# Kernel optimization log

Hardware: AMD Instinct MI355X
Metric: run time of the kernel (lower is better)

The kernel has to match this reference:

```python
import math
import jax, jax.numpy as jnp
import numpy as np

T = 4096          # sequence length
H = 2048          # hidden_size
I = 8192          # intermediate_size = 4*H
LAYER_ID = 1
N_LAYERS = 24
EPS = 1e-5        # layer_norm_epsilon


def setup_inputs() -> dict:
    key = jax.random.key(0)
    ks = jax.random.split(key, 8)
    s = 1.0 / math.sqrt(H)
    si = 1.0 / math.sqrt(I)
    r0 = LAYER_ID / (N_LAYERS - 1)          # ratio_0_to_1
    r1 = 1.0 - LAYER_ID / N_LAYERS          # ratio_1_to_almost_0
    h = jnp.arange(H, dtype=jnp.float32)
    x = h / H
    time_decay = -5.0 + 8.0 * (h / (H - 1)) ** (0.7 + 1.3 * r0)
    zigzag = 0.5 * ((jnp.arange(1, H + 1) % 3).astype(jnp.float32) - 1.0)
    time_first = jnp.full((H,), math.log(0.3), jnp.float32) + zigzag
    tm_key = x ** r1
    tm_value = tm_key + 0.3 * r0
    tm_recep = x ** (0.5 * r1)
    return {
        "hidden": jax.random.normal(ks[0], (T, H), jnp.float32),
        "att_sx": jnp.zeros((H,), jnp.float32),
        "att_aa": jnp.zeros((H,), jnp.float32),
        "att_bb": jnp.zeros((H,), jnp.float32),
        "att_pp": jnp.full((H,), -1e30, jnp.float32),  # log-space -inf init
        "ffd_sx": jnp.zeros((H,), jnp.float32),
        "ln1_scale": jnp.ones((H,), jnp.float32),
        "ln1_bias": jnp.zeros((H,), jnp.float32),
        "ln2_scale": jnp.ones((H,), jnp.float32),
        "ln2_bias": jnp.zeros((H,), jnp.float32),
        "time_decay": time_decay.astype(jnp.float32),
        "time_first": time_first,
        "tm_key": tm_key.astype(jnp.float32),
        "tm_value": tm_value.astype(jnp.float32),
        "tm_recep": tm_recep.astype(jnp.float32),
        "Wk": jax.random.normal(ks[1], (H, H), jnp.float32) * s,
        "Wv": jax.random.normal(ks[2], (H, H), jnp.float32) * s,
        "Wr": jax.random.normal(ks[3], (H, H), jnp.float32) * s,
        "Wo": jax.random.normal(ks[4], (H, H), jnp.float32) * s,
        "ffn_tm_key": (x ** r1).astype(jnp.float32),
        "ffn_tm_recep": (x ** (0.5 * r1)).astype(jnp.float32),
        "Wfk": jax.random.normal(ks[5], (H, I), jnp.float32) * s,
        "Wfr": jax.random.normal(ks[6], (H, H), jnp.float32) * s,
        "Wfv": jax.random.normal(ks[7], (I, H), jnp.float32) * si,
    }


def _ln(x, scale, bias):
    mu = jnp.mean(x, axis=-1, keepdims=True)
    var = jnp.mean(jnp.square(x - mu), axis=-1, keepdims=True)
    return (x - mu) * jax.lax.rsqrt(var + EPS) * scale + bias


def _block(hidden, att_sx, att_aa, att_bb, att_pp, ffd_sx,
           ln1_scale, ln1_bias, ln2_scale, ln2_bias,
           time_decay, time_first, tm_key, tm_value, tm_recep,
           Wk, Wv, Wr, Wo, ffn_tm_key, ffn_tm_recep, Wfk, Wfr, Wfv):
    # ---- attention (WKV) sub-block ----
    x1 = _ln(hidden, ln1_scale, ln1_bias)               # [T,H]
    c_x = jnp.concatenate((att_sx[None, :], x1[:-1, :]), axis=0)  # token shift
    kx = x1 * tm_key + c_x * (1.0 - tm_key)
    vx = x1 * tm_value + c_x * (1.0 - tm_value)
    rx = x1 * tm_recep + c_x * (1.0 - tm_recep)
    r = jax.nn.sigmoid(rx @ Wr)                         # [T,H]
    k = kx @ Wk
    v = vx @ Wv
    w_decay = -jnp.exp(time_decay)                      # [H]

    def step(carry, kv):
        aa, bb, pp = carry
        kk, vv = kv
        ww = time_first + kk
        p = jnp.maximum(pp, ww)
        e1 = jnp.exp(pp - p)
        e2 = jnp.exp(ww - p)
        out_t = (e1 * aa + e2 * vv) / (e1 * bb + e2)
        ww2 = w_decay + pp
        p2 = jnp.maximum(ww2, kk)
        e1b = jnp.exp(ww2 - p2)
        e2b = jnp.exp(kk - p2)
        return (e1b * aa + e2b * vv, e1b * bb + e2b, p2), out_t

    (aa, bb, pp), cx = jax.lax.scan(step, (att_aa, att_bb, att_pp), (k, v))
    attention = x1 + (r * cx) @ Wo                      # inner residual (as in source)
    hidden2 = hidden + attention

    # ---- feed-forward (channel-mix) sub-block ----
    x2 = _ln(hidden2, ln2_scale, ln2_bias)
    sx2 = jnp.concatenate((ffd_sx[None, :], x2[:-1, :]), axis=0)
    fk = x2 * ffn_tm_key + sx2 * (1.0 - ffn_tm_key)
    fr = x2 * ffn_tm_recep + sx2 * (1.0 - ffn_tm_recep)
    rr = jax.nn.sigmoid(fr @ Wfr)
    kk2 = jnp.square(jax.nn.relu(fk @ Wfk))             # [T,I]
    ffn = rr * (kk2 @ Wfv)
    out = hidden2 + ffn
    return out, x1[-1, :], aa, bb, pp, x2[-1, :]


def reference(hidden, att_sx, att_aa, att_bb, att_pp, ffd_sx,
              ln1_scale, ln1_bias, ln2_scale, ln2_bias,
              time_decay, time_first, tm_key, tm_value, tm_recep,
              Wk, Wv, Wr, Wo, ffn_tm_key, ffn_tm_recep, Wfk, Wfr, Wfv):
    return _block(hidden, att_sx, att_aa, att_bb, att_pp, ffd_sx,
                  ln1_scale, ln1_bias, ln2_scale, ln2_bias,
                  time_decay, time_first, tm_key, tm_value, tm_recep,
                  Wk, Wv, Wr, Wo, ffn_tm_key, ffn_tm_recep, Wfk, Wfr, Wfv)
```

## Files before the change

kernel.cpp:

```cpp
#include <hip/hip_runtime.h>

#define T_SEQ 4096
#define HD 2048
#define ID 8192
#define LN_EPS 1e-5f
#define NCH 64
#define CHL 64
#define CHSZ ((size_t)NCH * HD)

typedef __attribute__((ext_vector_type(4))) float f32x4;
typedef __attribute__((ext_vector_type(8))) short short8;
typedef __attribute__((ext_vector_type(4))) unsigned short ushort4v;

#define GLB(p) ((const __attribute__((address_space(1))) void*)(p))
#define LDSP(p) ((__attribute__((address_space(3))) void*)(p))

__device__ __forceinline__ unsigned short f2bf(float f) {
  union { float f; unsigned int u; } x; x.f = f;
  unsigned int r = x.u + 0x7fffu + ((x.u >> 16) & 1u);
  return (unsigned short)(r >> 16);
}
__device__ __forceinline__ float bf2f(unsigned short u) {
  union { unsigned int i; float f; } x; x.i = ((unsigned int)u) << 16;
  return x.f;
}

__global__ void k_wt(const float* __restrict__ W, unsigned short* __restrict__ Wt,
                     int Nfull, int k_base, int n_base, int Kout) {
  __shared__ float tile[32][33];
  int tx = threadIdx.x, ty = threadIdx.y;
  int n0 = blockIdx.x * 32, k0 = blockIdx.y * 32;
#pragma unroll
  for (int j = 0; j < 4; ++j) {
    int k = ty + 8 * j;
    tile[k][tx] = W[(size_t)(k_base + k0 + k) * Nfull + n_base + n0 + tx];
  }
  __syncthreads();
#pragma unroll
  for (int j = 0; j < 4; ++j) {
    int n = ty + 8 * j;
    Wt[(size_t)(n0 + n) * Kout + k0 + tx] = f2bf(tile[tx][n]);
  }
}

__global__ void k_ln(const float* __restrict__ x, const float* __restrict__ sc,
                     const float* __restrict__ bi, unsigned short* __restrict__ y,
                     float* __restrict__ lastrow) {
  int row = blockIdx.x, tid = threadIdx.x;
  const float* xr = x + (size_t)row * HD;
  f32x4 v0 = *(const f32x4*)(xr + tid * 4);
  f32x4 v1 = *(const f32x4*)(xr + 1024 + tid * 4);
  float s = 0.f, s2 = 0.f;
#pragma unroll
  for (int q = 0; q < 4; ++q) { s += v0[q] + v1[q]; s2 += v0[q] * v0[q] + v1[q] * v1[q]; }
#pragma unroll
  for (int o = 32; o; o >>= 1) { s += __shfl_xor(s, o); s2 += __shfl_xor(s2, o); }
  __shared__ float red[8];
  int wv = tid >> 6;
  if ((tid & 63) == 0) { red[wv] = s; red[4 + wv] = s2; }
  __syncthreads();
  if (tid == 0) {
    float a = red[0] + red[1] + red[2] + red[3];
    float b = red[4] + red[5] + red[6] + red[7];
    float mu = a * (1.f / HD);
    float var = b * (1.f / HD) - mu * mu;
    red[0] = mu; red[1] = rsqrtf(var + LN_EPS);
  }
  __syncthreads();
  float mu = red[0], rs = red[1];
  f32x4 s0 = *(const f32x4*)(sc + tid * 4), s1 = *(const f32x4*)(sc + 1024 + tid * 4);
  f32x4 b0 = *(const f32x4*)(bi + tid * 4), b1 = *(const f32x4*)(bi + 1024 + tid * 4);
  float o0[4], o1[4];
  ushort4v y0, y1;
#pragma unroll
  for (int q = 0; q < 4; ++q) {
    o0[q] = (v0[q] - mu) * rs * s0[q] + b0[q];
    o1[q] = (v1[q] - mu) * rs * s1[q] + b1[q];
    y0[q] = f2bf(o0[q]); y1[q] = f2bf(o1[q]);
  }
  unsigned short* yr = y + (size_t)row * HD;
  *(ushort4v*)(yr + tid * 4) = y0;
  *(ushort4v*)(yr + 1024 + tid * 4) = y1;
  if (row == T_SEQ - 1) {
#pragma unroll
    for (int q = 0; q < 4; ++q) {
      lastrow[tid * 4 + q] = o0[q];
      lastrow[1024 + tid * 4 + q] = o1[q];
    }
  }
}

__global__ void k_mix_att(const unsigned short* __restrict__ x1, const float* __restrict__ sx,
                          const float* __restrict__ tk, const float* __restrict__ tv,
                          const float* __restrict__ tr,
                          unsigned short* __restrict__ kx, unsigned short* __restrict__ vx,
                          unsigned short* __restrict__ rx) {
  size_t idx = ((size_t)blockIdx.x * 256 + threadIdx.x) * 4;
  int h = (int)(idx & (HD - 1));
  ushort4v xu = *(const ushort4v*)(x1 + idx);
  f32x4 x, c;
#pragma unroll
  for (int q = 0; q < 4; ++q) x[q] = bf2f(xu[q]);
  if (idx >= HD) {
    ushort4v cu = *(const ushort4v*)(x1 + idx - HD);
#pragma unroll
    for (int q = 0; q < 4; ++q) c[q] = bf2f(cu[q]);
  } else {
    c = *(const f32x4*)(sx + h);
  }
  f32x4 a = *(const f32x4*)(tk + h);
  f32x4 b = *(const f32x4*)(tv + h);
  f32x4 r = *(const f32x4*)(tr + h);
  ushort4v ok, ov, orr;
#pragma unroll
  for (int q = 0; q < 4; ++q) {
    ok[q] = f2bf(x[q] * a[q] + c[q] * (1.f - a[q]));
    ov[q] = f2bf(x[q] * b[q] + c[q] * (1.f - b[q]));
    orr[q] = f2bf(x[q] * r[q] + c[q] * (1.f - r[q]));
  }
  *(ushort4v*)(kx + idx) = ok;
  *(ushort4v*)(vx + idx) = ov;
  *(ushort4v*)(rx + idx) = orr;
}

__global__ void k_mix_ffn(const unsigned short* __restrict__ x2, const float* __restrict__ sx,
                          const float* __restrict__ tk, const float* __restrict__ tr,
                          unsigned short* __restrict__ fk, unsigned short* __restrict__ fr) {
  size_t idx = ((size_t)blockIdx.x * 256 + threadIdx.x) * 4;
  int h = (int)(idx & (HD - 1));
  ushort4v xu = *(const ushort4v*)(x2 + idx);
  f32x4 x, c;
#pragma unroll
  for (int q = 0; q < 4; ++q) x[q] = bf2f(xu[q]);
  if (idx >= HD) {
    ushort4v cu = *(const ushort4v*)(x2 + idx - HD);
#pragma unroll
    for (int q = 0; q < 4; ++q) c[q] = bf2f(cu[q]);
  } else {
    c = *(const f32x4*)(sx + h);
  }
  f32x4 a = *(const f32x4*)(tk + h);
  f32x4 r = *(const f32x4*)(tr + h);
  ushort4v ok, orr;
#pragma unroll
  for (int q = 0; q < 4; ++q) {
    ok[q] = f2bf(x[q] * a[q] + c[q] * (1.f - a[q]));
    orr[q] = f2bf(x[q] * r[q] + c[q] * (1.f - r[q]));
  }
  *(ushort4v*)(fk + idx) = ok;
  *(ushort4v*)(fr + idx) = orr;
}

__global__ void k_scan1(const unsigned short* __restrict__ kb,
                        const unsigned short* __restrict__ vb,
                        const float* __restrict__ td, float* __restrict__ scr) {
  int c = blockIdx.x >> 3;
  int h = (blockIdx.x & 7) * 256 + threadIdx.x;
  float wd = -__expf(td[h]);
  float a = 0.f, b = 0.f, p = -1e30f;
  size_t base = (size_t)c * CHL * HD + h;
#pragma unroll 4
  for (int u = 0; u < CHL; ++u) {
    float kk = bf2f(kb[base]), vv = bf2f(vb[base]);
    base += HD;
    float ww2 = wd + p;
    float p2 = fmaxf(ww2, kk);
    float e1 = __expf(ww2 - p2), e2 = __expf(kk - p2);
    a = e1 * a + e2 * vv;
    b = e1 * b + e2;
    p = p2;
  }
  size_t i = (size_t)c * HD + h;
  scr[i] = a;
  scr[CHSZ + i] = b;
  scr[2 * CHSZ + i] = p;
}

__global__ void k_scan2(const float* __restrict__ scr, float* __restrict__ stscr,
                        const float* __restrict__ aa0, const float* __restrict__ bb0,
                        const float* __restrict__ pp0, const float* __restrict__ td,
                        float* __restrict__ st) {
  int h = blockIdx.x * 256 + threadIdx.x;
  float aa = aa0[h], bb = bb0[h], pp = pp0[h];
  float wdL = -__expf(td[h]) * (float)CHL;
  for (int c = 0; c < NCH; ++c) {
    size_t i = (size_t)c * HD + h;
    stscr[i] = aa;
    stscr[CHSZ + i] = bb;
    stscr[2 * CHSZ + i] = pp;
    float ca = scr[i], cb = scr[CHSZ + i], cp = scr[2 * CHSZ + i];
    float ww2 = wdL + pp;
    float p2 = fmaxf(ww2, cp);
    float e1 = __expf(ww2 - p2), e2 = __expf(cp - p2);
    aa = e1 * aa + e2 * ca;
    bb = e1 * bb + e2 * cb;
    pp = p2;
  }
  st[HD + h] = aa;
  st[2 * HD + h] = bb;
  st[3 * HD + h] = pp;
}

__global__ void k_scan3(const unsigned short* __restrict__ kb,
                        const unsigned short* __restrict__ vb,
                        const unsigned short* __restrict__ rb,
                        const float* __restrict__ tf_, const float* __restrict__ td,
                        const float* __restrict__ stscr, unsigned short* __restrict__ rcx) {
  int c = blockIdx.x >> 3;
  int h = (blockIdx.x & 7) * 256 + threadIdx.x;
  size_t i0 = (size_t)c * HD + h;
  float aa = stscr[i0], bb = stscr[CHSZ + i0], pp = stscr[2 * CHSZ + i0];
  float tf = tf_[h];
  float wd = -__expf(td[h]);
  size_t base = (size_t)c * CHL * HD + h;
#pragma unroll 4
  for (int u = 0; u < CHL; ++u) {
    float kk = bf2f(kb[base]), vv = bf2f(vb[base]), rv = bf2f(rb[base]);
    float ww = tf + kk;
    float p = fmaxf(pp, ww);
    float e1 = __expf(pp - p), e2 = __expf(ww - p);
    float cx = (e1 * aa + e2 * vv) / (e1 * bb + e2);
    rcx[base] = f2bf(rv * cx);
    float ww2 = wd + pp;
    float p2 = fmaxf(ww2, kk);
    float e1b = __expf(ww2 - p2), e2b = __expf(kk - p2);
    aa = e1b * aa + e2b * vv;
    bb = e1b * bb + e2b;
    pp = p2;
    base += HD;
  }
}

#define MFMA_Q(mh, nh, bset)                                                   \
  _Pragma("unroll") for (int i_ = 0; i_ < 4; ++i_)                             \
  _Pragma("unroll") for (int j_ = 0; j_ < 2; ++j_)                             \
  _Pragma("unroll") for (int ks_ = 0; ks_ < 2; ++ks_)                          \
    acc[(mh)*4 + i_][(nh)*2 + j_] = __builtin_amdgcn_mfma_f32_16x16x32_bf16(   \
        aS[i_ * 2 + ks_], bset[j_ * 2 + ks_], acc[(mh)*4 + i_][(nh)*2 + j_], 0, 0, 0);

#define RD_A(mh)                                                               \
  { const char* pa_ = Ab + arow0 + (mh)*8192;                                  \
    aS[0] = *(const short8*)(pa_ + 0 * 2048 + swz0);                           \
    aS[1] = *(const short8*)(pa_ + 0 * 2048 + swz1);                           \
    aS[2] = *(const short8*)(pa_ + 1 * 2048 + swz0);                           \
    aS[3] = *(const short8*)(pa_ + 1 * 2048 + swz1);                           \
    aS[4] = *(const short8*)(pa_ + 2 * 2048 + swz0);                           \
    aS[5] = *(const short8*)(pa_ + 2 * 2048 + swz1);                           \
    aS[6] = *(const short8*)(pa_ + 3 * 2048 + swz0);                           \
    aS[7] = *(const short8*)(pa_ + 3 * 2048 + swz1); }

#define RD_B(arr, nh)                                                          \
  { const char* pb_ = Bb + brow0 + (nh)*4096;                                  \
    arr[0] = *(const short8*)(pb_ + 0 * 2048 + swz0);                          \
    arr[1] = *(const short8*)(pb_ + 0 * 2048 + swz1);                          \
    arr[2] = *(const short8*)(pb_ + 1 * 2048 + swz0);                          \
    arr[3] = *(const short8*)(pb_ + 1 * 2048 + swz1); }

template <int EPI>
__global__ __launch_bounds__(512, 2) void k_gemm256(
    const unsigned short* __restrict__ A, const unsigned short* __restrict__ A1,
    const unsigned short* __restrict__ A2,
    const unsigned short* __restrict__ Bt, const unsigned short* __restrict__ Bt1,
    const unsigned short* __restrict__ Bt2,
    int M, int N, int K, int lda,
    unsigned short* __restrict__ Cb, unsigned short* __restrict__ Cb1,
    unsigned short* __restrict__ Cb2) {
  if (blockIdx.z == 1) { A = A1; Bt = Bt1; Cb = Cb1; }
  else if (blockIdx.z == 2) { A = A2; Bt = Bt2; Cb = Cb2; }
  __shared__ char lds[131072];
  int tid = threadIdx.x;
  int wid = tid >> 6, lane = tid & 63;
  int row_l = lane & 15, kg = lane >> 4;
  int warp_m = wid >> 2, warp_n = wid & 3;
  int m0 = blockIdx.x * 256, n0 = blockIdx.y * 256;

  f32x4 acc[8][4];
#pragma unroll
  for (int i = 0; i < 8; ++i)
#pragma unroll
    for (int j = 0; j < 4; ++j)
#pragma unroll
      for (int q = 0; q < 4; ++q) acc[i][j][q] = 0.f;

  int srow = tid >> 3;
  int schunk = (tid & 7) ^ (srow & 7);
  const unsigned short* Asrc = A + (size_t)(m0 + srow) * lda + schunk * 8;
  const unsigned short* Bsrc = Bt + (size_t)(n0 + srow) * K + schunk * 8;
  char* ldsw = lds + wid * 1024;

  auto STAGE_TILE = [&](int d, int kt) {
#pragma unroll
    for (int h = 0; h < 2; ++h) {
      const unsigned short* s = Asrc + (size_t)(h * 128) * lda + kt;
      char* dst = ldsw + d * 65536 + h * 16384;
      __builtin_amdgcn_global_load_lds(GLB(s), LDSP(dst), 16, 0, 0);
      __builtin_amdgcn_global_load_lds(GLB(s + (size_t)64 * lda), LDSP(dst + 8192), 16, 0, 0);
    }
#pragma unroll
    for (int h = 0; h < 2; ++h) {
      const unsigned short* s = Bsrc + (size_t)(h * 128) * K + kt;
      char* dst = ldsw + d * 65536 + 32768 + h * 16384;
      __builtin_amdgcn_global_load_lds(GLB(s), LDSP(dst), 16, 0, 0);
      __builtin_amdgcn_global_load_lds(GLB(s + (size_t)64 * K), LDSP(dst + 8192), 16, 0, 0);
    }
  };

  int swz0 = ((kg) ^ (row_l & 7)) << 4;
  int swz1 = ((4 + kg) ^ (row_l & 7)) << 4;
  int arow0 = (warp_m * 128 + row_l) * 128;
  int brow0 = (warp_n * 64 + row_l) * 128;

  short8 aS[8], b0[4], b1[4];
  int nt = K >> 6;
  STAGE_TILE(0, 0);

#pragma unroll 1
  for (int t = 0; t < nt; ++t) {
    int d = t & 1;
    const char* Ab = lds + d * 65536;
    const char* Bb = lds + d * 65536 + 32768;
    bool pre = (t + 1 < nt);
    if (pre) {
      STAGE_TILE(d ^ 1, (t + 1) << 6);
      asm volatile("s_waitcnt vmcnt(8)" ::: "memory");
    } else {
      asm volatile("s_waitcnt vmcnt(0)" ::: "memory");
    }
    __builtin_amdgcn_s_barrier();
    RD_A(0)
    RD_B(b0, 0)
    asm volatile("s_waitcnt lgkmcnt(0)" ::: "memory");
    __builtin_amdgcn_s_setprio(1);
    MFMA_Q(0, 0, b0)
    __builtin_amdgcn_s_setprio(0);
    __builtin_amdgcn_s_barrier();
    RD_B(b1, 1)
    asm volatile("s_waitcnt lgkmcnt(0)" ::: "memory");
    __builtin_amdgcn_s_setprio(1);
    MFMA_Q(0, 1, b1)
    __builtin_amdgcn_s_setprio(0);
    __builtin_amdgcn_s_barrier();
    RD_A(1)
    asm volatile("s_waitcnt lgkmcnt(0)" ::: "memory");
    __builtin_amdgcn_s_setprio(1);
    MFMA_Q(1, 1, b1)
    __builtin_amdgcn_s_setprio(0);
    __builtin_amdgcn_s_barrier();
    __builtin_amdgcn_s_setprio(1);
    MFMA_Q(1, 0, b0)
    __builtin_amdgcn_s_setprio(0);
    __builtin_amdgcn_s_barrier();
  }

#pragma unroll
  for (int i = 0; i < 8; ++i) {
#pragma unroll
    for (int j = 0; j < 4; ++j) {
#pragma unroll
      for (int q = 0; q < 4; ++q) {
        int r = m0 + warp_m * 128 + i * 16 + kg * 4 + q;
        int c = n0 + warp_n * 64 + j * 16 + row_l;
        size_t idx = (size_t)r * N + c;
        float val = acc[i][j][q];
        if (EPI == 2) { float t2 = val > 0.f ? val * val : 0.f; Cb[idx] = f2bf(t2); }
        if (EPI == 8) {
          float o = (blockIdx.z == 2) ? 1.f / (1.f + __expf(-val)) : val;
          Cb[idx] = f2bf(o);
        }
      }
    }
  }
}

template <int EPI>
__global__ __launch_bounds__(256) void k_gemm(
    const unsigned short* __restrict__ A, const unsigned short* __restrict__ Bt,
    int M, int N, int K, int lda, float* __restrict__ C,
    unsigned short* __restrict__ Cb, const float* __restrict__ E0,
    const unsigned short* __restrict__ E1b, const unsigned short* __restrict__ E0b) {
  __shared__ unsigned short As[3][128 * 32];
  __shared__ unsigned short Bs[3][128 * 32];
  int tid = threadIdx.x;
  int wave = tid >> 6, lane = tid & 63;
  int row_l = lane & 15, kg = lane >> 4;
  int m0 = blockIdx.x * 128, n0 = blockIdx.y * 128;
  int wm = (wave >> 1) * 64, wn = (wave & 1) * 64;
  f32x4 acc[4][4];
#pragma unroll
  for (int i = 0; i < 4; ++i)
#pragma unroll
    for (int j = 0; j < 4; ++j)
#pragma unroll
      for (int q = 0; q < 4; ++q) acc[i][j][q] = 0.f;

  int trow = tid >> 2, tcol = (tid & 3) * 8;
  const unsigned short* Ag = A + (size_t)(m0 + trow) * lda + tcol;
  const unsigned short* Bg = Bt + (size_t)(n0 + trow) * K + tcol;
  size_t rhalfA = (size_t)64 * lda;
  size_t rhalfB = (size_t)64 * K;
  int woff = wave * 1024;
  int nk = K >> 5;

  auto STAGE = [&](int t, int b) {
    int kt = t * 32;
    char* ad = (char*)As + b * 8192 + woff;
    char* bd = (char*)Bs + b * 8192 + woff;
    __builtin_amdgcn_global_load_lds(GLB(Ag + kt), LDSP(ad), 16, 0, 0);
    __builtin_amdgcn_global_load_lds(GLB(Ag + rhalfA + kt), LDSP(ad + 4096), 16, 0, 0);
    __builtin_amdgcn_global_load_lds(GLB(Bg + kt), LDSP(bd), 16, 0, 0);
    __builtin_amdgcn_global_load_lds(GLB(Bg + rhalfB + kt), LDSP(bd + 4096), 16, 0, 0);
  };

  STAGE(0, 0);
  STAGE(1, 1);
  int buf = 0;
  for (int t = 0; t < nk; ++t) {
    if (t + 2 < nk) {
      int b2 = buf + 2; if (b2 >= 3) b2 -= 3;
      STAGE(t + 2, b2);
      asm volatile("s_waitcnt vmcnt(8)" ::: "memory");
    } else if (t + 1 < nk) {
      asm volatile("s_waitcnt vmcnt(4)" ::: "memory");
    } else {
      asm volatile("s_waitcnt vmcnt(0)" ::: "memory");
    }
    __builtin_amdgcn_s_barrier();
    const unsigned short* Ab = As[buf];
    const unsigned short* Bb = Bs[buf];
    short8 af[4], bfv[4];
#pragma unroll
    for (int i = 0; i < 4; ++i)
      af[i] = *(const short8*)(Ab + (wm + i * 16 + row_l) * 32 + kg * 8);
#pragma unroll
    for (int j = 0; j < 4; ++j)
      bfv[j] = *(const short8*)(Bb + (wn + j * 16 + row_l) * 32 + kg * 8);
    __builtin_amdgcn_s_setprio(1);
#pragma unroll
    for (int i = 0; i < 4; ++i)
#pragma unroll
      for (int j = 0; j < 4; ++j)
        acc[i][j] = __builtin_amdgcn_mfma_f32_16x16x32_bf16(af[i], bfv[j], acc[i][j], 0, 0, 0);
    __builtin_amdgcn_s_setprio(0);
    asm volatile("s_waitcnt lgkmcnt(0)" ::: "memory");
    __builtin_amdgcn_s_barrier();
    ++buf; if (buf >= 3) buf -= 3;
  }

#pragma unroll
  for (int i = 0; i < 4; ++i) {
#pragma unroll
    for (int j = 0; j < 4; ++j) {
#pragma unroll
      for (int q = 0; q < 4; ++q) {
        int r = m0 + wm + i * 16 + kg * 4 + q;
        int c = n0 + wn + j * 16 + row_l;
        size_t idx = (size_t)r * N + c;
        float val = acc[i][j][q];
        if (EPI == 3) C[idx] = val + E0[idx] + bf2f(E1b[idx]);
        if (EPI == 6) Cb[idx] = f2bf(1.f / (1.f + __expf(-val)));
        if (EPI == 7) C[idx] += bf2f(E0b[idx]) * val;
      }
    }
  }
}

extern "C" void kernel_launch(void* const* d_in, const int* in_sizes, int n_in,
                              void* d_out, int out_size, void* d_ws, size_t ws_size,
                              hipStream_t stream) {
  (void)in_sizes; (void)n_in; (void)out_size; (void)ws_size;
  const float* hidden     = (const float*)d_in[0];
  const float* att_sx     = (const float*)d_in[1];
  const float* att_aa     = (const float*)d_in[2];
  const float* att_bb     = (const float*)d_in[3];
  const float* att_pp     = (const float*)d_in[4];
  const float* ffd_sx     = (const float*)d_in[5];
  const float* ln1_s      = (const float*)d_in[6];
  const float* ln1_b      = (const float*)d_in[7];
  const float* ln2_s      = (const float*)d_in[8];
  const float* ln2_b      = (const float*)d_in[9];
  const float* time_decay = (const float*)d_in[10];
  const float* time_first = (const float*)d_in[11];
  const float* tm_key     = (const float*)d_in[12];
  const float* tm_value   = (const float*)d_in[13];
  const float* tm_recep   = (const float*)d_in[14];
  const float* Wk         = (const float*)d_in[15];
  const float* Wv         = (const float*)d_in[16];
  const float* Wr         = (const float*)d_in[17];
  const float* Wo         = (const float*)d_in[18];
  const float* ffn_tm_key = (const float*)d_in[19];
  const float* ffn_tm_rec = (const float*)d_in[20];
  const float* Wfk        = (const float*)d_in[21];
  const float* Wfr        = (const float*)d_in[22];
  const float* Wfv        = (const float*)d_in[23];
  float* out = (float*)d_out;
  float* st = out + (size_t)T_SEQ * HD;

  const size_t MB8 = (size_t)HD * HD * 2;
  const size_t PG = (size_t)T_SEQ * HD * 2;
  char* w = (char*)d_ws;
  unsigned short* s0 = (unsigned short*)(w);
  unsigned short* s1 = (unsigned short*)(w + MB8);
  unsigned short* s2 = (unsigned short*)(w + 2 * MB8);
  unsigned short* s3 = (unsigned short*)(w + 3 * MB8);
  char* pA = w + 4 * MB8;
  char* pB = pA + PG;
  char* pC = pB + PG;
  char* pD = pC + PG;
  char* pE = pD + PG;
  char* pF = pE + PG;

  unsigned short* kx   = (unsigned short*)pA;
  unsigned short* vx   = (unsigned short*)pB;
  unsigned short* rx   = (unsigned short*)pC;
  unsigned short* kbf  = (unsigned short*)pD;
  unsigned short* x1bf = (unsigned short*)pE;
  unsigned short* vbf  = (unsigned short*)pF;
  unsigned short* rbf  = (unsigned short*)out;
  unsigned short* rcx  = (unsigned short*)pC;
  unsigned short* x2bf = (unsigned short*)pD;
  unsigned short* fk   = (unsigned short*)pF;
  unsigned short* fr   = (unsigned short*)pB;
  unsigned short* rr   = (unsigned short*)pA;
  unsigned short* kk2  = (unsigned short*)pB;
  float* scr   = (float*)s0;
  float* stscr = (float*)s1;

  dim3 tb(32, 8);
  dim3 wg64(HD / 32, HD / 32);
  dim3 gg(T_SEQ / 128, HD / 128);

  k_wt<<<wg64, tb, 0, stream>>>(Wk, s0, HD, 0, 0, HD);
  k_wt<<<wg64, tb, 0, stream>>>(Wv, s1, HD, 0, 0, HD);
  k_wt<<<wg64, tb, 0, stream>>>(Wr, s2, HD, 0, 0, HD);
  k_wt<<<wg64, tb, 0, stream>>>(Wo, s3, HD, 0, 0, HD);
  k_ln<<<T_SEQ, 256, 0, stream>>>(hidden, ln1_s, ln1_b, x1bf, st);
  k_mix_att<<<T_SEQ * HD / 1024, 256, 0, stream>>>(x1bf, att_sx, tm_key, tm_value, tm_recep,
                                                   kx, vx, rx);
  k_gemm256<8><<<dim3(T_SEQ / 256, HD / 256, 3), 512, 0, stream>>>(
      kx, vx, rx, s0, s1, s2, T_SEQ, HD, HD, HD, kbf, vbf, rbf);
  k_scan1<<<NCH * 8, 256, 0, stream>>>(kbf, vbf, time_decay, scr);
  k_scan2<<<HD / 256, 256, 0, stream>>>(scr, stscr, att_aa, att_bb, att_pp, time_decay, st);
  k_scan3<<<NCH * 8, 256, 0, stream>>>(kbf, vbf, rbf, time_first, time_decay, stscr, rcx);
  k_gemm<3><<<gg, 256, 0, stream>>>(rcx, s3, T_SEQ, HD, HD, HD, out, nullptr,
                                    hidden, x1bf, nullptr);

  k_ln<<<T_SEQ, 256, 0, stream>>>(out, ln2_s, ln2_b, x2bf, st + 4 * HD);
  k_mix_ffn<<<T_SEQ * HD / 1024, 256, 0, stream>>>(x2bf, ffd_sx, ffn_tm_key, ffn_tm_rec,
                                                   fk, fr);
  k_wt<<<wg64, tb, 0, stream>>>(Wfr, s3, HD, 0, 0, HD);
  k_gemm<6><<<gg, 256, 0, stream>>>(fr, s3, T_SEQ, HD, HD, HD, nullptr, rr,
                                    nullptr, nullptr, nullptr);
  for (int q = 0; q < 4; ++q)
    k_wt<<<wg64, tb, 0, stream>>>(Wfk, s0 + (size_t)q * 2048 * 2048, ID, 0, q * 2048, HD);
  k_gemm256<2><<<dim3(T_SEQ / 256, ID / 256), 512, 0, stream>>>(
      fk, nullptr, nullptr, s0, nullptr, nullptr, T_SEQ, ID, HD, HD,
      kk2, nullptr, nullptr);
  for (int q = 0; q < 4; ++q)
    k_wt<<<dim3(HD / 32, HD / 32), tb, 0, stream>>>(Wfv, s0 + (size_t)q * 2048, HD,
                                                    q * 2048, 0, ID);
  k_gemm<7><<<gg, 256, 0, stream>>>(kk2, s0, T_SEQ, HD, ID, ID, out, nullptr,
                                    nullptr, nullptr, rr);
}
```

Baseline: 736.2 us.

## Replace 128x128 GEMM with 128x256 tile, 512-thread, swizzled LDS variant

The three N=2048 GEMMs (attention output, FFN receptance, FFN value) move to a new kernel that uses 128x256 output tiles with 8 waves and K-steps of 64. It double-buffers in place of triple-buffering and applies an XOR swizzle to the LDS layout to avoid bank conflicts, reusing the RD_A/RD_B/MFMA_Q macros from the 256 kernel. The larger tile raises arithmetic intensity per LDS load, but halves the grid to 256 blocks, which may leave some of the 256 CUs underused or unevenly loaded. The bigger LDS footprint (96KB) also limits occupancy to one block per CU.

After: 674.7 us. 8.4% less time.

```diff
diff --git a/kernel.cpp b/kernel.cpp
--- a/kernel.cpp
+++ b/kernel.cpp
@@ -373,18 +373,18 @@
 }
 
 template <int EPI>
-__global__ __launch_bounds__(256) void k_gemm(
+__global__ __launch_bounds__(512) void k_gemmB(
     const unsigned short* __restrict__ A, const unsigned short* __restrict__ Bt,
     int M, int N, int K, int lda, float* __restrict__ C,
     unsigned short* __restrict__ Cb, const float* __restrict__ E0,
     const unsigned short* __restrict__ E1b, const unsigned short* __restrict__ E0b) {
-  __shared__ unsigned short As[3][128 * 32];
-  __shared__ unsigned short Bs[3][128 * 32];
+  __shared__ char lds[98304];
   int tid = threadIdx.x;
-  int wave = tid >> 6, lane = tid & 63;
+  int wid = tid >> 6, lane = tid & 63;
   int row_l = lane & 15, kg = lane >> 4;
-  int m0 = blockIdx.x * 128, n0 = blockIdx.y * 128;
-  int wm = (wave >> 1) * 64, wn = (wave & 1) * 64;
+  int warp_m = wid >> 2, warp_n = wid & 3;
+  int m0 = blockIdx.x * 128, n0 = blockIdx.y * 256;
+
   f32x4 acc[4][4];
 #pragma unroll
   for (int i = 0; i < 4; ++i)
@@ -393,57 +393,57 @@
 #pragma unroll
       for (int q = 0; q < 4; ++q) acc[i][j][q] = 0.f;
 
-  int trow = tid >> 2, tcol = (tid & 3) * 8;
-  const unsigned short* Ag = A + (size_t)(m0 + trow) * lda + tcol;
-  const unsigned short* Bg = Bt + (size_t)(n0 + trow) * K + tcol;
-  size_t rhalfA = (size_t)64 * lda;
-  size_t rhalfB = (size_t)64 * K;
-  int woff = wave * 1024;
-  int nk = K >> 5;
-
-  auto STAGE = [&](int t, int b) {
-    int kt = t * 32;
-    char* ad = (char*)As + b * 8192 + woff;
-    char* bd = (char*)Bs + b * 8192 + woff;
-    __builtin_amdgcn_global_load_lds(GLB(Ag + kt), LDSP(ad), 16, 0, 0);
-    __builtin_amdgcn_global_load_lds(GLB(Ag + rhalfA + kt), LDSP(ad + 4096), 16, 0, 0);
-    __builtin_amdgcn_global_load_lds(GLB(Bg + kt), LDSP(bd), 16, 0, 0);
-    __builtin_amdgcn_global_load_lds(GLB(Bg + rhalfB + kt), LDSP(bd + 4096), 16, 0, 0);
+  int srow = tid >> 3;
+  int schunk = (tid & 7) ^ (srow & 7);
+  const unsigned short* Asrc = A + (size_t)(m0 + srow) * lda + schunk * 8;
+  const unsigned short* Bsrc = Bt + (size_t)(n0 + srow) * K + schunk * 8;
+  int wsw = wid * 1024;
+
+  auto STAGE_TILE = [&](int d, int kt) {
+    char* base = lds + d * 49152;
+    __builtin_amdgcn_global_load_lds(GLB(Asrc + kt), LDSP(base + wsw), 16, 0, 0);
+    __builtin_amdgcn_global_load_lds(GLB(Asrc + (size_t)64 * lda + kt),
+                                     LDSP(base + 8192 + wsw), 16, 0, 0);
+#pragma unroll
+    for (int h = 0; h < 4; ++h)
+      __builtin_amdgcn_global_load_lds(GLB(Bsrc + (size_t)(h * 64) * K + kt),
+                                       LDSP(base + 16384 + h * 8192 + wsw), 16, 0, 0);
   };
 
-  STAGE(0, 0);
-  STAGE(1, 1);
-  int buf = 0;
-  for (int t = 0; t < nk; ++t) {
-    if (t + 2 < nk) {
-      int b2 = buf + 2; if (b2 >= 3) b2 -= 3;
-      STAGE(t + 2, b2);
-      asm volatile("s_waitcnt vmcnt(8)" ::: "memory");
-    } else if (t + 1 < nk) {
-      asm volatile("s_waitcnt vmcnt(4)" ::: "memory");
+  int swz0 = ((kg) ^ (row_l & 7)) << 4;
+  int swz1 = ((4 + kg) ^ (row_l & 7)) << 4;
+  int arow0 = (warp_m * 64 + row_l) * 128;
+  int brow0 = (warp_n * 64 + row_l) * 128;
+
+  short8 aS[8], b0[4], b1[4];
+  int nt = K >> 6;
+  STAGE_TILE(0, 0);
+
+#pragma unroll 1
+  for (int t = 0; t < nt; ++t) {
+    int d = t & 1;
+    const char* Ab = lds + d * 49152;
+    const char* Bb = lds + d * 49152 + 16384;
+    if (t + 1 < nt) {
+      STAGE_TILE(d ^ 1, (t + 1) << 6);
+      asm volatile("s_waitcnt vmcnt(6)" ::: "memory");
     } else {
       asm volatile("s_waitcnt vmcnt(0)" ::: "memory");
     }
     __builtin_amdgcn_s_barrier();
-    const unsigned short* Ab = As[buf];
-    const unsigned short* Bb = Bs[buf];
-    short8 af[4], bfv[4];
-#pragma unroll
-    for (int i = 0; i < 4; ++i)
-      af[i] = *(const short8*)(Ab + (wm + i * 16 + row_l) * 32 + kg * 8);
-#pragma unroll
-    for (int j = 0; j < 4; ++j)
-      bfv[j] = *(const short8*)(Bb + (wn + j * 16 + row_l) * 32 + kg * 8);
+    RD_A(0)
+    RD_B(b0, 0)
+    asm volatile("s_waitcnt lgkmcnt(0)" ::: "memory");
     __builtin_amdgcn_s_setprio(1);
-#pragma unroll
-    for (int i = 0; i < 4; ++i)
-#pragma unroll
-      for (int j = 0; j < 4; ++j)
-        acc[i][j] = __builtin_amdgcn_mfma_f32_16x16x32_bf16(af[i], bfv[j], acc[i][j], 0, 0, 0);
+    MFMA_Q(0, 0, b0)
     __builtin_amdgcn_s_setprio(0);
+    __builtin_amdgcn_s_barrier();
+    RD_B(b1, 1)
     asm volatile("s_waitcnt lgkmcnt(0)" ::: "memory");
-    __builtin_amdgcn_s_barrier();
-    ++buf; if (buf >= 3) buf -= 3;
+    __builtin_amdgcn_s_setprio(1);
+    MFMA_Q(0, 1, b1)
+    __builtin_amdgcn_s_setprio(0);
+    __builtin_amdgcn_s_barrier();
   }
 
 #pragma unroll
@@ -452,8 +452,8 @@
     for (int j = 0; j < 4; ++j) {
 #pragma unroll
       for (int q = 0; q < 4; ++q) {
-        int r = m0 + wm + i * 16 + kg * 4 + q;
-        int c = n0 + wn + j * 16 + row_l;
+        int r = m0 + warp_m * 64 + i * 16 + kg * 4 + q;
+        int c = n0 + warp_n * 64 + j * 16 + row_l;
         size_t idx = (size_t)r * N + c;
         float val = acc[i][j][q];
         if (EPI == 3) C[idx] = val + E0[idx] + bf2f(E1b[idx]);
@@ -527,7 +527,7 @@
 
   dim3 tb(32, 8);
   dim3 wg64(HD / 32, HD / 32);
-  dim3 gg(T_SEQ / 128, HD / 128);
+  dim3 gB(T_SEQ / 128, HD / 256);
 
   k_wt<<<wg64, tb, 0, stream>>>(Wk, s0, HD, 0, 0, HD);
   k_wt<<<wg64, tb, 0, stream>>>(Wv, s1, HD, 0, 0, HD);
@@ -541,15 +541,15 @@
   k_scan1<<<NCH * 8, 256, 0, stream>>>(kbf, vbf, time_decay, scr);
   k_scan2<<<HD / 256, 256, 0, stream>>>(scr, stscr, att_aa, att_bb, att_pp, time_decay, st);
   k_scan3<<<NCH * 8, 256, 0, stream>>>(kbf, vbf, rbf, time_first, time_decay, stscr, rcx);
-  k_gemm<3><<<gg, 256, 0, stream>>>(rcx, s3, T_SEQ, HD, HD, HD, out, nullptr,
-                                    hidden, x1bf, nullptr);
+  k_gemmB<3><<<gB, 512, 0, stream>>>(rcx, s3, T_SEQ, HD, HD, HD, out, nullptr,
+                                     hidden, x1bf, nullptr);
 
   k_ln<<<T_SEQ, 256, 0, stream>>>(out, ln2_s, ln2_b, x2bf, st + 4 * HD);
   k_mix_ffn<<<T_SEQ * HD / 1024, 256, 0, stream>>>(x2bf, ffd_sx, ffn_tm_key, ffn_tm_rec,
                                                    fk, fr);
   k_wt<<<wg64, tb, 0, stream>>>(Wfr, s3, HD, 0, 0, HD);
-  k_gemm<6><<<gg, 256, 0, stream>>>(fr, s3, T_SEQ, HD, HD, HD, nullptr, rr,
-                                    nullptr, nullptr, nullptr);
+  k_gemmB<6><<<gB, 512, 0, stream>>>(fr, s3, T_SEQ, HD, HD, HD, nullptr, rr,
+                                     nullptr, nullptr, nullptr);
   for (int q = 0; q < 4; ++q)
     k_wt<<<wg64, tb, 0, stream>>>(Wfk, s0 + (size_t)q * 2048 * 2048, ID, 0, q * 2048, HD);
   k_gemm256<2><<<dim3(T_SEQ / 256, ID / 256), 512, 0, stream>>>(
@@ -558,6 +558,6 @@
   for (int q = 0; q < 4; ++q)
     k_wt<<<dim3(HD / 32, HD / 32), tb, 0, stream>>>(Wfv, s0 + (size_t)q * 2048, HD,
                                                     q * 2048, 0, ID);
-  k_gemm<7><<<gg, 256, 0, stream>>>(kk2, s0, T_SEQ, HD, ID, ID, out, nullptr,
-                                    nullptr, nullptr, rr);
-}
+  k_gemmB<7><<<gB, 512, 0, stream>>>(kk2, s0, T_SEQ, HD, ID, ID, out, nullptr,
+                                     nullptr, nullptr, rr);
+}
```
